# Kernel tuning notes

Measured on AMD Instinct MI355X. Metric: run time of the kernel, lower is better.

## Reference

```python
import jax, jax.numpy as jnp
import numpy as np

RES = 32          # resolution (32, 32) -> N = 1024 tokens
HEADS = 16
EMB = 1024
BATCH = 8
N = RES * RES


def _bias_idxs(res):
    # relative-offset index table, [N, N] with values in [0, res*res)
    coords = np.stack(np.meshgrid(np.arange(res), np.arange(res), indexing='ij'), -1).reshape(-1, 2)
    d = np.abs(coords[:, None, :] - coords[None, :, :])  # [N, N, 2]
    return jnp.asarray(d[..., 0] * res + d[..., 1], dtype=jnp.int64)


def setup_inputs() -> dict:
    key = jax.random.key(0)
    k1, k2, k3, k4, k5 = jax.random.split(key, 5)
    x = jax.random.normal(k1, (BATCH, N, EMB), dtype=jnp.float32)
    w_qkv = jax.random.normal(k2, (3 * EMB, EMB), dtype=jnp.float32) * 0.02
    biases = jax.random.normal(k3, (HEADS, RES * RES), dtype=jnp.float32) * 0.02
    bias_idxs = _bias_idxs(RES)
    w_out = jax.random.normal(k4, (EMB, EMB), dtype=jnp.float32) * 0.02
    b_out = jax.random.normal(k5, (EMB,), dtype=jnp.float32) * 0.02
    return {"x": x, "w_qkv": w_qkv, "biases": biases,
            "bias_idxs": bias_idxs, "w_out": w_out, "b_out": b_out}


def reference(x, w_qkv, biases, bias_idxs, w_out, b_out):
    b, n, e = x.shape
    h = HEADS
    d = e // h
    scale = d ** -0.5
    # to_qkv: Linear(e, 3e, bias=False); torch Linear computes x @ W.T
    qkv = x @ w_qkv.T                                   # [b, n, 3e]
    q, k, v = jnp.split(qkv, 3, axis=-1)
    def to_heads(t):
        return t.reshape(b, n, h, d).transpose(0, 2, 1, 3)  # b h n d
    q, k, v = to_heads(q), to_heads(k), to_heads(v)
    scores = jnp.einsum('bhid,bhjd->bhij', q, k) * scale    # [b, h, n, n]
    scores = scores + biases[:, bias_idxs]                  # gather -> [h, n, n], broadcast over b
    attn = jax.nn.softmax(scores, axis=-1)
    out = jnp.einsum('bhij,bhjd->bhid', attn, v)            # [b, h, n, d]
    out = out.transpose(0, 2, 1, 3).reshape(b, n, e)        # b n (h d)
    # to_out: Linear(e, e) with bias (dropout = identity at inference)
    return out @ w_out.T + b_out
```

## Files before the change

kernel.cpp:

```cpp
#include <hip/hip_runtime.h>
#include <stdint.h>


#define LOG2E 1.4426950408889634f
#define QSCL 0.18033688011112042f

typedef __attribute__((ext_vector_type(8))) short short8;
typedef __attribute__((ext_vector_type(4))) short short4v;
typedef __attribute__((ext_vector_type(4))) float floatx4;
typedef __attribute__((ext_vector_type(2))) unsigned int uint2v;

__device__ __forceinline__ short f2bf(float f) {
  uint32_t u = __builtin_bit_cast(uint32_t, f);
  u = (u + 0x7FFFu + ((u >> 16) & 1u)) >> 16;
  return (short)(uint16_t)u;
}
__device__ __forceinline__ float bf2f(short s) {
  uint32_t u = ((uint32_t)(uint16_t)s) << 16;
  return __builtin_bit_cast(float, u);
}
__device__ __forceinline__ float fast_exp2(float x) {
#if __has_builtin(__builtin_amdgcn_exp2f)
  return __builtin_amdgcn_exp2f(x);
#else
  return exp2f(x);
#endif
}

__device__ __forceinline__ void gload_lds16(const short* g, short* l) {
  __builtin_amdgcn_global_load_lds(
      (const __attribute__((address_space(1))) void*)g,
      (__attribute__((address_space(3))) void*)l, 16, 0, 0);
}

__global__ void prep(const float* __restrict__ x, const float* __restrict__ wqkv,
                     const float* __restrict__ wout, const float* __restrict__ biases,
                     short* __restrict__ xb, short* __restrict__ wqkvb,
                     short* __restrict__ woutb, short* __restrict__ biast) {
  int blk = blockIdx.x, tid = threadIdx.x;
  if (blk < 12288) {
    const float* src;
    short* dst;
    int i;
    if (blk < 8192) { src = x; dst = xb; i = blk * 256 + tid; }
    else if (blk < 11264) { src = wqkv; dst = wqkvb; i = (blk - 8192) * 256 + tid; }
    else { src = wout; dst = woutb; i = (blk - 11264) * 256 + tid; }
    float4 f = ((const float4*)src)[i];
    short4v o;
    o.x = f2bf(f.x); o.y = f2bf(f.y); o.z = f2bf(f.z); o.w = f2bf(f.w);
    ((short4v*)dst)[i] = o;
  } else {
    int tile = (blk - 12288) * 4 + (tid >> 6);
    int lane = tid & 63, qd = lane >> 4, col = lane & 15;
    int bp = tile & 1, ap = (tile >> 1) & 1, dra = (tile >> 2) & 31, h = tile >> 7;
    int ci = 16 * bp + col;
    short4v o;
#pragma unroll
    for (int r = 0; r < 4; r++) {
      int cj = 16 * ap + 4 * qd + r;
      int dc = cj - ci; if (dc < 0) dc = -dc;
      o[r] = f2bf(biases[h * 1024 + dra * 32 + dc] * LOG2E);
    }
    *(short4v*)&biast[(size_t)tile * 256 + lane * 4] = o;
  }
}

template <int MODE>
__global__ __launch_bounds__(256, 3) void gemm_bt(
    const short* __restrict__ A, const short* __restrict__ Bt,
    short* __restrict__ qo, short* __restrict__ ko, short* __restrict__ vto,
    const float* __restrict__ bvec, float* __restrict__ outf) {
  __shared__ __align__(16) short sA[128 * 64];
  __shared__ __align__(16) short sB[128 * 64];
  const int tid = threadIdx.x;
  const int w = tid >> 6, lane = tid & 63;
  const int wr = w >> 1, wc = w & 1;
  const int bm = blockIdx.y, bn = blockIdx.x;
  const int qd = lane >> 4, col = lane & 15;

  floatx4 acc[4][4] = {};
  const int rowA0 = bm * 128, rowB0 = bn * 128;
  const int ciw = w * 256;

  for (int kk = 0; kk < 1024; kk += 64) {
    __syncthreads();
#pragma unroll
    for (int n = 0; n < 4; n++) {
      int ci = ciw + n * 64 + lane;
      int r = ci >> 3, c = (ci & 7) ^ (r & 7);
      gload_lds16(A + (size_t)(rowA0 + r) * 1024 + kk + c * 8, &sA[ci * 8]);
    }
#pragma unroll
    for (int n = 0; n < 4; n++) {
      int ci = ciw + n * 64 + lane;
      int r = ci >> 3, c = (ci & 7) ^ (r & 7);
      gload_lds16(Bt + (size_t)(rowB0 + r) * 1024 + kk + c * 8, &sB[ci * 8]);
    }
    __syncthreads();

#pragma unroll
    for (int ks = 0; ks < 2; ks++) {
      const int ch = qd + ks * 4;
      short8 af[4], bff[4];
#pragma unroll
      for (int rt = 0; rt < 4; rt++) {
        int r = wr * 64 + rt * 16 + col;
        af[rt] = *(const short8*)&sA[r * 64 + ((ch ^ (r & 7)) << 3)];
      }
#pragma unroll
      for (int ct = 0; ct < 4; ct++) {
        int r = wc * 64 + ct * 16 + col;
        bff[ct] = *(const short8*)&sB[r * 64 + ((ch ^ (r & 7)) << 3)];
      }
#pragma unroll
      for (int rt = 0; rt < 4; rt++)
#pragma unroll
        for (int ct = 0; ct < 4; ct++)
          acc[rt][ct] = __builtin_amdgcn_mfma_f32_16x16x32_bf16(af[rt], bff[ct], acc[rt][ct], 0, 0, 0);
    }
  }

  if (MODE == 0) {
    if (bn >= 16) {
#pragma unroll
      for (int rt = 0; rt < 4; rt++) {
#pragma unroll
        for (int ct = 0; ct < 4; ct++) {
          int Cg = bn * 128 + wc * 64 + ct * 16 + col;
          int e = Cg & 1023, h = e >> 6, dd = e & 63;
          short4v pv;
#pragma unroll
          for (int r = 0; r < 4; r++) pv[r] = f2bf(acc[rt][ct][r]);
          int R0 = bm * 128 + wr * 64 + rt * 16 + qd * 4;
          int b = R0 >> 10, n0 = R0 & 1023;
          int bh = b * 16 + h;
          *(short4v*)&vto[((size_t)bh * 64 + dd) * 1024 + n0] = pv;
        }
      }
    } else {
#pragma unroll
      for (int rt = 0; rt < 4; rt++) {
#pragma unroll
        for (int ct = 0; ct < 4; ct++) {
          int Cg = bn * 128 + wc * 64 + ct * 16 + col;
          int which = Cg >> 10, e = Cg & 1023, h = e >> 6, dd = e & 63;
#pragma unroll
          for (int r = 0; r < 4; r++) {
            int R = bm * 128 + wr * 64 + rt * 16 + qd * 4 + r;
            int b = R >> 10, n = R & 1023;
            int bh = b * 16 + h;
            float av = acc[rt][ct][r];
            if (which == 0) av *= QSCL;
            short v = f2bf(av);
            if (which == 0)
              qo[((size_t)bh * 1024 + n) * 64 + dd] = v;
            else
              ko[((size_t)bh * 1024 + n) * 64 + dd] = v;
          }
        }
      }
    }
  } else {
#pragma unroll
    for (int rt = 0; rt < 4; rt++)
#pragma unroll
      for (int ct = 0; ct < 4; ct++) {
        int Cg = bn * 128 + wc * 64 + ct * 16 + col;
        float bo = bvec[Cg];
#pragma unroll
        for (int r = 0; r < 4; r++) {
          int R = bm * 128 + wr * 64 + rt * 16 + qd * 4 + r;
          outf[(size_t)R * 1024 + Cg] = acc[rt][ct][r] + bo;
        }
      }
  }
}

__global__ __launch_bounds__(256, 3) void attn_fused(
    const short* __restrict__ q, const short* __restrict__ k,
    const short* __restrict__ vt, const short* __restrict__ biast,
    short* __restrict__ ao) {
  __shared__ __align__(16) short sK[128 * 64];
  __shared__ __align__(16) short sVt[64 * 128];
  __shared__ __align__(16) short sP[64 * 128];
  const int tid = threadIdx.x, w = tid >> 6, lane = tid & 63;
  const int bh = blockIdx.x, qt = blockIdx.y;
  const int h = bh & 15;
  const int qd = lane >> 4, col = lane & 15;
  const short* qb = q + (size_t)bh * 65536;
  const short* kb = k + (size_t)bh * 65536;
  const short* vb = vt + (size_t)bh * 65536;
  const int ciw = w * 256;

#pragma unroll
  for (int n = 0; n < 2; n++) {
    int ci = w * 128 + n * 64 + lane;
    int r = ci >> 3, c = (ci & 7) ^ (r & 7);
    gload_lds16(qb + (size_t)(qt * 64 + r) * 64 + c * 8, &sP[ci * 8]);
  }
  __syncthreads();
  short8 bq[2][4];
#pragma unroll
  for (int ks = 0; ks < 2; ks++) {
    const int ch = qd + ks * 4;
#pragma unroll
    for (int ct = 0; ct < 4; ct++) {
      int r2 = ct * 16 + col;
      bq[ks][ct] = *(const short8*)&sP[r2 * 64 + ((ch ^ (r2 & 7)) << 3)];
    }
  }

  short8 onesf;
#pragma unroll
  for (int t = 0; t < 8; t++) onesf[t] = (short)0x3F80;

  floatx4 oacc[4] = {};
  floatx4 osum = {};

  for (int js = 0; js < 8; js++) {
    __syncthreads();

    short4v bfrag[2][4];
#pragma unroll
    for (int rt = 0; rt < 2; rt++) {
      const int a = js * 8 + w * 2 + rt;
      const int ar = a >> 1, ap = a & 1;
#pragma unroll
      for (int ct = 0; ct < 4; ct++) {
        int b = qt * 4 + ct;
        int dra = ar - (b >> 1); if (dra < 0) dra = -dra;
        int tile = ((h * 32 + dra) * 2 + ap) * 2 + (b & 1);
        bfrag[rt][ct] = *(const short4v*)&biast[(size_t)tile * 256 + lane * 4];
      }
    }

#pragma unroll
    for (int n = 0; n < 4; n++) {
      int ci = ciw + n * 64 + lane;
      int r = ci >> 3, c = (ci & 7) ^ (r & 7);
      gload_lds16(kb + (size_t)(js * 128 + r) * 64 + c * 8, &sK[ci * 8]);
    }
#pragma unroll
    for (int n = 0; n < 4; n++) {
      int ci = ciw + n * 64 + lane;
      int r = ci >> 4, c = (ci & 15) ^ (r & 15);
      gload_lds16(vb + (size_t)r * 1024 + js * 128 + c * 8, &sVt[ci * 8]);
    }
    __syncthreads();

#pragma unroll
    for (int rt = 0; rt < 2; rt++) {
      const int s = w * 8 + rt * 4 + qd;
      const int r = w * 32 + rt * 16 + col;
      short8 ak0 = *(const short8*)&sK[r * 64 + (((qd + 0) ^ (r & 7)) << 3)];
      short8 ak1 = *(const short8*)&sK[r * 64 + (((qd + 4) ^ (r & 7)) << 3)];
      floatx4 sacc[4];
#pragma unroll
      for (int ct = 0; ct < 4; ct++) {
        sacc[ct][0] = bf2f(bfrag[rt][ct][0]);
        sacc[ct][1] = bf2f(bfrag[rt][ct][1]);
        sacc[ct][2] = bf2f(bfrag[rt][ct][2]);
        sacc[ct][3] = bf2f(bfrag[rt][ct][3]);
      }
      __builtin_amdgcn_s_setprio(1);
#pragma unroll
      for (int ct = 0; ct < 4; ct++)
        sacc[ct] = __builtin_amdgcn_mfma_f32_16x16x32_bf16(ak0, bq[0][ct], sacc[ct], 0, 0, 0);
#pragma unroll
      for (int ct = 0; ct < 4; ct++)
        sacc[ct] = __builtin_amdgcn_mfma_f32_16x16x32_bf16(ak1, bq[1][ct], sacc[ct], 0, 0, 0);
      __builtin_amdgcn_s_setprio(0);
#pragma unroll
      for (int ct = 0; ct < 4; ct++) {
        int i = ct * 16 + col;
        float e0 = fast_exp2(sacc[ct][0]);
        float e1 = fast_exp2(sacc[ct][1]);
        float e2 = fast_exp2(sacc[ct][2]);
        float e3 = fast_exp2(sacc[ct][3]);
        uint32_t u0 = __builtin_bit_cast(uint32_t, e0) + 0x8000u;
        uint32_t u1 = __builtin_bit_cast(uint32_t, e1) + 0x8000u;
        uint32_t u2 = __builtin_bit_cast(uint32_t, e2) + 0x8000u;
        uint32_t u3 = __builtin_bit_cast(uint32_t, e3) + 0x8000u;
        uint2v pk;
        pk.x = __builtin_amdgcn_perm(u1, u0, 0x07060302u);
        pk.y = __builtin_amdgcn_perm(u3, u2, 0x07060302u);
        *(uint2v*)&sP[i * 128 + ((s ^ (i & 15)) << 2)] = pk;
      }
    }
    __syncthreads();

#pragma unroll
    for (int ks = 0; ks < 4; ks++) {
      const int ch = ks * 4 + qd;
      int m = w * 16 + col;
      short4v lo = *(const short4v*)&sP[m * 128 + (((2 * ch) ^ col) << 2)];
      short4v hi = *(const short4v*)&sP[m * 128 + (((2 * ch + 1) ^ col) << 2)];
      short8 ap = __builtin_shufflevector(lo, hi, 0, 1, 2, 3, 4, 5, 6, 7);
      short8 bv[4];
#pragma unroll
      for (int ct = 0; ct < 4; ct++) {
        int d = ct * 16 + col;
        bv[ct] = *(const short8*)&sVt[d * 128 + ((ch ^ (d & 15)) << 3)];
      }
      __builtin_amdgcn_s_setprio(1);
#pragma unroll
      for (int ct = 0; ct < 4; ct++)
        oacc[ct] = __builtin_amdgcn_mfma_f32_16x16x32_bf16(ap, bv[ct], oacc[ct], 0, 0, 0);
      osum = __builtin_amdgcn_mfma_f32_16x16x32_bf16(ap, onesf, osum, 0, 0, 0);
      __builtin_amdgcn_s_setprio(0);
    }
  }

  const int b = bh >> 4;
  floatx4 inv;
#pragma unroll
  for (int r = 0; r < 4; r++) inv[r] = 1.0f / osum[r];
#pragma unroll
  for (int ct = 0; ct < 4; ct++)
#pragma unroll
    for (int r = 0; r < 4; r++) {
      int n = qt * 64 + w * 16 + qd * 4 + r;
      int dd = ct * 16 + col;
      ao[(((size_t)b * 1024 + n) << 10) + h * 64 + dd] = f2bf(oacc[ct][r] * inv[r]);
    }
}

extern "C" void kernel_launch(void* const* d_in, const int* in_sizes, int n_in,
                              void* d_out, int out_size, void* d_ws, size_t ws_size,
                              hipStream_t stream) {
  const float* x = (const float*)d_in[0];
  const float* w_qkv = (const float*)d_in[1];
  const float* biases = (const float*)d_in[2];
  const float* w_out = (const float*)d_in[4];
  const float* b_out = (const float*)d_in[5];
  float* out = (float*)d_out;

  char* ws = (char*)d_ws;
  short* xb    = (short*)(ws + 0);
  short* wqkvb = (short*)(ws + 16777216);
  short* woutb = (short*)(ws + 23068672);
  short* qb    = (short*)(ws + 25165824);
  short* kb    = (short*)(ws + 41943040);
  short* vtb   = (short*)(ws + 58720256);
  short* aob   = (short*)(ws + 75497472);
  short* biast = (short*)(ws + 92274688);

  prep<<<13312, 256, 0, stream>>>(x, w_qkv, w_out, biases, xb, wqkvb, woutb, biast);
  gemm_bt<0><<<dim3(24, 64), 256, 0, stream>>>(xb, wqkvb, qb, kb, vtb, nullptr, nullptr);
  attn_fused<<<dim3(128, 16), 256, 0, stream>>>(qb, kb, vtb, biast, aob);
  gemm_bt<1><<<dim3(8, 64), 256, 0, stream>>>(aob, woutb, nullptr, nullptr, nullptr, b_out, out);
}
```

Measured before the change: 236.4 us.

## Keep softmax probabilities in registers and split PV over keys across waves

The attention kernel no longer writes exponentiated scores to a shared-memory P tile and reads them back. Each wave now keeps its P fragment in registers as the MFMA A operand and accumulates a partial output over its own key slice for all 64 queries. Row sums are kept as scalar register sums instead of an extra ones-MFMA. The four per-wave partial outputs and row sums are reduced through shared memory in an epilogue. This drops the sP buffer and one barrier per key tile, and cuts LDS from 48KB to 32KB. In exchange it uses 64 accumulator registers, which may lower occupancy, and adds a multi-stage reduction at the end.

```diff
diff --git a/kernel.cpp b/kernel.cpp
--- a/kernel.cpp
+++ b/kernel.cpp
@@ -9,6 +9,7 @@
 typedef __attribute__((ext_vector_type(4))) short short4v;
 typedef __attribute__((ext_vector_type(4))) float floatx4;
 typedef __attribute__((ext_vector_type(2))) unsigned int uint2v;
+typedef __attribute__((ext_vector_type(4))) unsigned int uint4v;
 
 __device__ __forceinline__ short f2bf(float f) {
   uint32_t u = __builtin_bit_cast(uint32_t, f);
@@ -180,9 +181,9 @@
     const short* __restrict__ q, const short* __restrict__ k,
     const short* __restrict__ vt, const short* __restrict__ biast,
     short* __restrict__ ao) {
-  __shared__ __align__(16) short sK[128 * 64];
-  __shared__ __align__(16) short sVt[64 * 128];
-  __shared__ __align__(16) short sP[64 * 128];
+  __shared__ __align__(16) short smem[16384];
+  short* sK = smem;
+  short* sVt = smem + 8192;
   const int tid = threadIdx.x, w = tid >> 6, lane = tid & 63;
   const int bh = blockIdx.x, qt = blockIdx.y;
   const int h = bh & 15;
@@ -196,7 +197,7 @@
   for (int n = 0; n < 2; n++) {
     int ci = w * 128 + n * 64 + lane;
     int r = ci >> 3, c = (ci & 7) ^ (r & 7);
-    gload_lds16(qb + (size_t)(qt * 64 + r) * 64 + c * 8, &sP[ci * 8]);
+    gload_lds16(qb + (size_t)(qt * 64 + r) * 64 + c * 8, &sK[ci * 8]);
   }
   __syncthreads();
   short8 bq[2][4];
@@ -206,61 +207,52 @@
 #pragma unroll
     for (int ct = 0; ct < 4; ct++) {
       int r2 = ct * 16 + col;
-      bq[ks][ct] = *(const short8*)&sP[r2 * 64 + ((ch ^ (r2 & 7)) << 3)];
-    }
-  }
-
-  short8 onesf;
-#pragma unroll
-  for (int t = 0; t < 8; t++) onesf[t] = (short)0x3F80;
-
-  floatx4 oacc[4] = {};
-  floatx4 osum = {};
+      bq[ks][ct] = *(const short8*)&sK[r2 * 64 + ((ch ^ (r2 & 7)) << 3)];
+    }
+  }
+  __syncthreads();
+
+  floatx4 oacc[4][4] = {};
+  float rs[4] = {0.f, 0.f, 0.f, 0.f};
 
   for (int js = 0; js < 8; js++) {
+#pragma unroll
+    for (int n = 0; n < 4; n++) {
+      int ci = ciw + n * 64 + lane;
+      int r = ci >> 3, c = (ci & 7) ^ (r & 7);
+      gload_lds16(kb + (size_t)(js * 128 + r) * 64 + c * 8, &sK[ci * 8]);
+    }
+#pragma unroll
+    for (int n = 0; n < 4; n++) {
+      int ci = ciw + n * 64 + lane;
+      int r = ci >> 4, c = (ci & 15) ^ (r & 15);
+      gload_lds16(vb + (size_t)r * 1024 + js * 128 + c * 8, &sVt[ci * 8]);
+    }
     __syncthreads();
 
-    short4v bfrag[2][4];
+    uint32_t pw[4][4];
 #pragma unroll
     for (int rt = 0; rt < 2; rt++) {
       const int a = js * 8 + w * 2 + rt;
       const int ar = a >> 1, ap = a & 1;
+      short4v bfrag[4];
 #pragma unroll
       for (int ct = 0; ct < 4; ct++) {
         int b = qt * 4 + ct;
         int dra = ar - (b >> 1); if (dra < 0) dra = -dra;
         int tile = ((h * 32 + dra) * 2 + ap) * 2 + (b & 1);
-        bfrag[rt][ct] = *(const short4v*)&biast[(size_t)tile * 256 + lane * 4];
-      }
-    }
-
-#pragma unroll
-    for (int n = 0; n < 4; n++) {
-      int ci = ciw + n * 64 + lane;
-      int r = ci >> 3, c = (ci & 7) ^ (r & 7);
-      gload_lds16(kb + (size_t)(js * 128 + r) * 64 + c * 8, &sK[ci * 8]);
-    }
-#pragma unroll
-    for (int n = 0; n < 4; n++) {
-      int ci = ciw + n * 64 + lane;
-      int r = ci >> 4, c = (ci & 15) ^ (r & 15);
-      gload_lds16(vb + (size_t)r * 1024 + js * 128 + c * 8, &sVt[ci * 8]);
-    }
-    __syncthreads();
-
-#pragma unroll
-    for (int rt = 0; rt < 2; rt++) {
-      const int s = w * 8 + rt * 4 + qd;
+        bfrag[ct] = *(const short4v*)&biast[(size_t)tile * 256 + lane * 4];
+      }
       const int r = w * 32 + rt * 16 + col;
       short8 ak0 = *(const short8*)&sK[r * 64 + (((qd + 0) ^ (r & 7)) << 3)];
       short8 ak1 = *(const short8*)&sK[r * 64 + (((qd + 4) ^ (r & 7)) << 3)];
       floatx4 sacc[4];
 #pragma unroll
       for (int ct = 0; ct < 4; ct++) {
-        sacc[ct][0] = bf2f(bfrag[rt][ct][0]);
-        sacc[ct][1] = bf2f(bfrag[rt][ct][1]);
-        sacc[ct][2] = bf2f(bfrag[rt][ct][2]);
-        sacc[ct][3] = bf2f(bfrag[rt][ct][3]);
+        sacc[ct][0] = bf2f(bfrag[ct][0]);
+        sacc[ct][1] = bf2f(bfrag[ct][1]);
+        sacc[ct][2] = bf2f(bfrag[ct][2]);
+        sacc[ct][3] = bf2f(bfrag[ct][3]);
       }
       __builtin_amdgcn_s_setprio(1);
 #pragma unroll
@@ -272,57 +264,115 @@
       __builtin_amdgcn_s_setprio(0);
 #pragma unroll
       for (int ct = 0; ct < 4; ct++) {
-        int i = ct * 16 + col;
         float e0 = fast_exp2(sacc[ct][0]);
         float e1 = fast_exp2(sacc[ct][1]);
         float e2 = fast_exp2(sacc[ct][2]);
         float e3 = fast_exp2(sacc[ct][3]);
+        rs[ct] += (e0 + e1) + (e2 + e3);
         uint32_t u0 = __builtin_bit_cast(uint32_t, e0) + 0x8000u;
         uint32_t u1 = __builtin_bit_cast(uint32_t, e1) + 0x8000u;
         uint32_t u2 = __builtin_bit_cast(uint32_t, e2) + 0x8000u;
         uint32_t u3 = __builtin_bit_cast(uint32_t, e3) + 0x8000u;
-        uint2v pk;
-        pk.x = __builtin_amdgcn_perm(u1, u0, 0x07060302u);
-        pk.y = __builtin_amdgcn_perm(u3, u2, 0x07060302u);
-        *(uint2v*)&sP[i * 128 + ((s ^ (i & 15)) << 2)] = pk;
-      }
-    }
+        pw[ct][2 * rt + 0] = __builtin_amdgcn_perm(u1, u0, 0x07060302u);
+        pw[ct][2 * rt + 1] = __builtin_amdgcn_perm(u3, u2, 0x07060302u);
+      }
+    }
+
+    short8 pa[4], bv[4];
+#pragma unroll
+    for (int ct = 0; ct < 4; ct++)
+      pa[ct] = __builtin_bit_cast(short8, (uint4v){pw[ct][0], pw[ct][1], pw[ct][2], pw[ct][3]});
+    const int jc0 = 4 * w + (qd >> 1), off = 4 * (qd & 1);
+#pragma unroll
+    for (int ct = 0; ct < 4; ct++) {
+      int d = ct * 16 + col;
+      short4v lo4 = *(const short4v*)&sVt[d * 128 + ((jc0 ^ (d & 15)) << 3) + off];
+      short4v hi4 = *(const short4v*)&sVt[d * 128 + (((jc0 + 2) ^ (d & 15)) << 3) + off];
+      bv[ct] = __builtin_shufflevector(lo4, hi4, 0, 1, 2, 3, 4, 5, 6, 7);
+    }
+    __builtin_amdgcn_s_setprio(1);
+#pragma unroll
+    for (int ci2 = 0; ci2 < 4; ci2++)
+#pragma unroll
+      for (int cd = 0; cd < 4; cd++)
+        oacc[ci2][cd] = __builtin_amdgcn_mfma_f32_16x16x32_bf16(pa[ci2], bv[cd], oacc[ci2][cd], 0, 0, 0);
+    __builtin_amdgcn_s_setprio(0);
     __syncthreads();
-
-#pragma unroll
-    for (int ks = 0; ks < 4; ks++) {
-      const int ch = ks * 4 + qd;
-      int m = w * 16 + col;
-      short4v lo = *(const short4v*)&sP[m * 128 + (((2 * ch) ^ col) << 2)];
-      short4v hi = *(const short4v*)&sP[m * 128 + (((2 * ch + 1) ^ col) << 2)];
-      short8 ap = __builtin_shufflevector(lo, hi, 0, 1, 2, 3, 4, 5, 6, 7);
-      short8 bv[4];
-#pragma unroll
-      for (int ct = 0; ct < 4; ct++) {
-        int d = ct * 16 + col;
-        bv[ct] = *(const short8*)&sVt[d * 128 + ((ch ^ (d & 15)) << 3)];
-      }
-      __builtin_amdgcn_s_setprio(1);
-#pragma unroll
-      for (int ct = 0; ct < 4; ct++)
-        oacc[ct] = __builtin_amdgcn_mfma_f32_16x16x32_bf16(ap, bv[ct], oacc[ct], 0, 0, 0);
-      osum = __builtin_amdgcn_mfma_f32_16x16x32_bf16(ap, onesf, osum, 0, 0, 0);
-      __builtin_amdgcn_s_setprio(0);
-    }
-  }
-
-  const int b = bh >> 4;
-  floatx4 inv;
-#pragma unroll
-  for (int r = 0; r < 4; r++) inv[r] = 1.0f / osum[r];
+  }
+
+  float* fs = (float*)smem;
 #pragma unroll
   for (int ct = 0; ct < 4; ct++)
-#pragma unroll
-    for (int r = 0; r < 4; r++) {
-      int n = qt * 64 + w * 16 + qd * 4 + r;
-      int dd = ct * 16 + col;
-      ao[(((size_t)b * 1024 + n) << 10) + h * 64 + dd] = f2bf(oacc[ct][r] * inv[r]);
-    }
+    fs[(w * 4 + qd) * 64 + 16 * ct + col] = rs[ct];
+  __syncthreads();
+  {
+    float tot = 0.f;
+#pragma unroll
+    for (int kk = 0; kk < 16; kk++) tot += fs[kk * 64 + lane];
+    fs[1024 + lane] = 1.0f / tot;
+  }
+  __syncthreads();
+  float myinv[8];
+  if (w < 2) {
+#pragma unroll
+    for (int t2 = 0; t2 < 2; t2++)
+#pragma unroll
+      for (int r = 0; r < 4; r++)
+        myinv[t2 * 4 + r] = fs[1024 + (w * 2 + t2) * 16 + 4 * qd + r];
+  }
+  __syncthreads();
+  if (w >= 2) {
+    float* ob = fs + (w - 2) * 4096;
+#pragma unroll
+    for (int ci2 = 0; ci2 < 4; ci2++)
+#pragma unroll
+      for (int cd = 0; cd < 4; cd++)
+        *(floatx4*)&ob[((ci2 * 4 + cd) * 64 + lane) * 4] = oacc[ci2][cd];
+  }
+  __syncthreads();
+  if (w < 2) {
+    float* ob = fs + w * 4096;
+#pragma unroll
+    for (int ci2 = 0; ci2 < 4; ci2++)
+#pragma unroll
+      for (int cd = 0; cd < 4; cd++)
+        oacc[ci2][cd] += *(const floatx4*)&ob[((ci2 * 4 + cd) * 64 + lane) * 4];
+  }
+  __syncthreads();
+  if (w == 1) {
+#pragma unroll
+    for (int t2 = 0; t2 < 2; t2++)
+#pragma unroll
+      for (int cd = 0; cd < 4; cd++)
+        *(floatx4*)&fs[((t2 * 4 + cd) * 64 + lane) * 4] = oacc[t2][cd];
+  }
+  if (w == 0) {
+#pragma unroll
+    for (int t2 = 0; t2 < 2; t2++)
+#pragma unroll
+      for (int cd = 0; cd < 4; cd++)
+        *(floatx4*)&fs[2048 + ((t2 * 4 + cd) * 64 + lane) * 4] = oacc[2 + t2][cd];
+  }
+  __syncthreads();
+  if (w < 2) {
+    const int b = bh >> 4;
+#pragma unroll
+    for (int t2 = 0; t2 < 2; t2++) {
+      int cti = w * 2 + t2;
+#pragma unroll
+      for (int cd = 0; cd < 4; cd++) {
+        floatx4 p = *(const floatx4*)&fs[w * 2048 + ((t2 * 4 + cd) * 64 + lane) * 4];
+        floatx4 o = oacc[cti][cd] + p;
+#pragma unroll
+        for (int r = 0; r < 4; r++) {
+          int i = 16 * cti + 4 * qd + r;
+          int n = qt * 64 + i;
+          int dd = cd * 16 + col;
+          ao[(((size_t)b * 1024 + n) << 10) + h * 64 + dd] = f2bf(o[r] * myinv[t2 * 4 + r]);
+        }
+      }
+    }
+  }
 }
 
 extern "C" void kernel_launch(void* const* d_in, const int* in_sizes, int n_in,
```

Measured after the change: 561.6 us. +137.5%, slower.
